# Optimization experiments

Hardware: AMD Instinct MI355X
Metric: run time of the kernel (lower is better)

## Reference

```python
import jax, jax.numpy as jnp
import numpy as np

NUM_HEADS = 8
NUM_LEVEL = 4
KERNEL = 2
NUM_POINT = KERNEL * KERNEL
D_MODEL = 256
HEAD_DIM = D_MODEL // NUM_HEADS
REF_SIZE = 4
EPS = 1e-6


def _kernel_indices():
    # even kernel: linspace(-k/2+0.5, k/2-0.5, k) -> [-0.5, 0.5] for k=2
    ind = np.linspace(-KERNEL // 2 + 0.5, KERNEL // 2 - 0.5, KERNEL)
    i, j = np.meshgrid(ind, ind, indexing='ij')
    ki = np.stack([j, i], axis=-1).reshape(-1, 2) / KERNEL  # (P, 2), (x, y)
    return jnp.asarray(ki, dtype=jnp.float32)


def _ref_windows(shapes):
    # mask is None -> centers on a regular grid, size = ref_size / (H, W)
    refs = []
    for (H, W) in shapes:
        y = (jnp.arange(1, H + 1, dtype=jnp.float32) - 0.5) / (H + EPS)
        x = (jnp.arange(1, W + 1, dtype=jnp.float32) - 0.5) / (W + EPS)
        yy, xx = jnp.meshgrid(y, x, indexing='ij')           # (H, W)
        center = jnp.stack([xx, yy], axis=-1).reshape(-1, 2)  # (HW, 2)
        size = jnp.broadcast_to(
            jnp.array([REF_SIZE / W, REF_SIZE / H], dtype=jnp.float32), center.shape)
        refs.append(jnp.concatenate([center, size], axis=-1))
    return jnp.concatenate(refs, axis=0)  # (L, 4)


def _bilinear_sample(vflat, grid, H, W):
    """vflat: (B, H*W, M, D) one level; grid: (B, Lq, M, P, 2) normalized [0,1].
    Returns (B, Lq, M, P, D). Zero padding outside, align_corners=False."""
    B, _, M, D = vflat.shape
    x = grid[..., 0] * W - 0.5
    y = grid[..., 1] * H - 0.5
    x0 = jnp.floor(x); y0 = jnp.floor(y)
    lx = x - x0; ly = y - y0
    x0i = x0.astype(jnp.int32); y0i = y0.astype(jnp.int32)
    bidx = jnp.arange(B)[:, None, None, None]
    midx = jnp.arange(M)[None, None, :, None]

    def corner(xi, yi, w):
        valid = (xi >= 0) & (xi < W) & (yi >= 0) & (yi < H)
        idx = jnp.clip(yi, 0, H - 1) * W + jnp.clip(xi, 0, W - 1)
        g = vflat[bidx, idx, midx]  # (B, Lq, M, P, D)
        return g * (w * valid.astype(w.dtype))[..., None]

    out = corner(x0i, y0i, (1 - lx) * (1 - ly))
    out = out + corner(x0i + 1, y0i, lx * (1 - ly))
    out = out + corner(x0i, y0i + 1, (1 - lx) * ly)
    out = out + corner(x0i + 1, y0i + 1, lx * ly)
    return out


def setup_inputs() -> dict:
    key = jax.random.key(0)
    ks = jax.random.split(key, 20)
    spatial = [(100, 100), (50, 50), (25, 25), (13, 13)]
    B = 4
    inp = {}
    for i, (H, W) in enumerate(spatial):
        inp[f'value{i}'] = jax.random.normal(ks[i], (B, D_MODEL, H, W), dtype=jnp.float32)
        inp[f'pos{i}'] = jax.random.normal(ks[4 + i], (B, D_MODEL, H, W), dtype=jnp.float32)
    s = 0.05
    inp['Wv'] = jax.random.normal(ks[8], (D_MODEL, D_MODEL), dtype=jnp.float32) * s
    inp['bv'] = jnp.zeros((D_MODEL,), dtype=jnp.float32)
    inp['Wo'] = jax.random.normal(ks[9], (D_MODEL, D_MODEL), dtype=jnp.float32) * s
    inp['bo'] = jnp.zeros((D_MODEL,), dtype=jnp.float32)
    nb = NUM_LEVEL * NUM_HEADS * 4
    inp['Wbox'] = jax.random.normal(ks[10], (nb, D_MODEL), dtype=jnp.float32) * s
    inp['bbox'] = jax.random.uniform(ks[11], (nb,), dtype=jnp.float32)
    na = NUM_HEADS * NUM_LEVEL * NUM_POINT
    inp['Wattn'] = jax.random.normal(ks[12], (na, D_MODEL), dtype=jnp.float32) * s
    inp['battn'] = jax.random.normal(ks[13], (na,), dtype=jnp.float32) * s
    return inp


def reference(value0, value1, value2, value3, pos0, pos1, pos2, pos3,
              Wv, bv, Wo, bo, Wbox, bbox, Wattn, battn):
    levels = [value0, value1, value2, value3]
    poss = [pos0, pos1, pos2, pos3]
    shapes = [(v.shape[2], v.shape[3]) for v in levels]
    B = levels[0].shape[0]

    # flatten pyramid: (B, C, H, W) -> (B, HW, C)
    value = jnp.concatenate(
        [v.reshape(B, D_MODEL, -1).transpose(0, 2, 1) for v in levels], axis=1)
    pos = jnp.concatenate(
        [p.reshape(B, D_MODEL, -1).transpose(0, 2, 1) for p in poss], axis=1)
    L = value.shape[1]

    query = value + pos
    vp = (value @ Wv.T + bv).reshape(B, L, NUM_HEADS, HEAD_DIM)

    attn = jax.nn.softmax(
        (query @ Wattn.T + battn).reshape(B, L, NUM_HEADS, NUM_LEVEL * NUM_POINT),
        axis=-1).reshape(B, L, NUM_HEADS, NUM_LEVEL, NUM_POINT)

    offset = (query @ Wbox.T + bbox).reshape(B, L, NUM_HEADS, NUM_LEVEL, 4)
    ref = _ref_windows(shapes)[None, :, None, None, :]          # (1, L, 1, 1, 4)
    boxes = ref + offset / 8.0 * ref[..., jnp.array([2, 3, 2, 3])]
    center = boxes[..., None, :2]                               # (B, L, M, NL, 1, 2)
    size = boxes[..., None, 2:]
    ki = _kernel_indices()[None, None, None, None, :, :]        # (1,1,1,1,P,2)
    grid = center + ki * jax.nn.relu(size)                      # (B, L, M, NL, P, 2)

    out = jnp.zeros((B, L, NUM_HEADS, HEAD_DIM), dtype=vp.dtype)
    start = 0
    for l, (H, W) in enumerate(shapes):
        end = start + H * W
        vf = vp[:, start:end]                                   # (B, HW, M, D)
        sampled = _bilinear_sample(vf, grid[:, :, :, l], H, W)  # (B, L, M, P, D)
        out = out + jnp.einsum('blmp,blmpd->blmd', attn[:, :, :, l], sampled)
        start = end

    return out.reshape(B, L, D_MODEL) @ Wo.T + bo
```

## Files before the change

### kernel.cpp

```cpp
#include <hip/hip_runtime.h>
#include <cstdint>
#include <cmath>

#define D_MODEL 256
#define NH 8
#define NLVL 4
#define LTOT 13294
#define BATCH 4
#define BTOT (BATCH * LTOT)
#define RPAD 53248

typedef __attribute__((ext_vector_type(8))) short bf8;
typedef __attribute__((ext_vector_type(4))) float f4;
typedef __attribute__((ext_vector_type(2))) float f2;

__device__ __forceinline__ unsigned short f2bf(float x) {
    unsigned u = __float_as_uint(x);
    u += 0x7fffu + ((u >> 16) & 1u);
    return (unsigned short)(u >> 16);
}
__device__ __forceinline__ float bf2f(unsigned short h) {
    return __uint_as_float(((unsigned)h) << 16);
}
__device__ __forceinline__ f2 up2(unsigned u) {
    return (f2){__uint_as_float(u << 16), __uint_as_float(u & 0xffff0000u)};
}
__device__ __forceinline__ int swzf(int i, int s) { return s ^ ((i >> 1) & 3); }

__device__ __forceinline__ void level_of(int l, int& lv, int& hw, int& Wl, int& HWl, int& loff) {
    if (l < 10000)      { lv = 0; loff = 0;     Wl = 100; HWl = 10000; }
    else if (l < 12500) { lv = 1; loff = 10000; Wl = 50;  HWl = 2500;  }
    else if (l < 13125) { lv = 2; loff = 12500; Wl = 25;  HWl = 625;   }
    else                { lv = 3; loff = 13125; Wl = 13;  HWl = 169;   }
    hw = l - loff;
}

__global__ __launch_bounds__(256) void pack_weights(
    const float* __restrict__ Wv, const float* __restrict__ Wattn,
    const float* __restrict__ Wbox, const float* __restrict__ Wo,
    unsigned short* __restrict__ W1hi, unsigned short* __restrict__ W1lo,
    unsigned short* __restrict__ Wohi, unsigned short* __restrict__ Wolo) {
    int tid = blockIdx.x * 256 + threadIdx.x;
    const float* src;
    unsigned short *dh, *dl;
    int nb, kb, j, s;
    if (tid < 16384) {
        nb = tid >> 12; kb = (tid >> 9) & 7; j = (tid >> 2) & 127; s = tid & 3;
        int f = nb * 128 + j, c0 = kb * 32 + s * 8;
        if (f < 256)      src = Wv + (size_t)f * 256 + c0;
        else if (f < 384) src = Wattn + (size_t)(f - 256) * 256 + c0;
        else              src = Wbox + (size_t)(f - 384) * 256 + c0;
        dh = W1hi; dl = W1lo;
    } else if (tid < 24576) {
        int t2 = tid - 16384;
        nb = t2 >> 12; kb = (t2 >> 9) & 7; j = (t2 >> 2) & 127; s = t2 & 3;
        int f = nb * 128 + j, c0 = kb * 32 + s * 8;
        src = Wo + (size_t)f * 256 + c0;
        dh = Wohi; dl = Wolo;
    } else return;
    int base = (((nb * 8 + kb) * 128 + j) * 4 + swzf(j, s)) * 8;
    #pragma unroll
    for (int e = 0; e < 8; ++e) {
        float x = src[e];
        unsigned short h = f2bf(x);
        dh[base + e] = h;
        dl[base + e] = f2bf(x - bf2f(h));
    }
}

__global__ __launch_bounds__(256) void convert_A(
    const float* __restrict__ v0, const float* __restrict__ v1,
    const float* __restrict__ v2, const float* __restrict__ v3,
    const float* __restrict__ p0, const float* __restrict__ p1,
    const float* __restrict__ p2, const float* __restrict__ p3,
    unsigned short* __restrict__ Gv, unsigned short* __restrict__ Gq) {
    __shared__ unsigned short HV[64][130];
    __shared__ unsigned short HQ[64][130];
    int t = threadIdx.x;
    int w = t >> 6, lane = t & 63;
    int r0 = blockIdx.x * 64;

    int r = r0 + lane; if (r >= BTOT) r = BTOT - 1;
    int b = r / LTOT, l = r % LTOT;
    int lv, hw, Wl, HWl, loff;
    level_of(l, lv, hw, Wl, HWl, loff);
    const float *vb, *pb;
    switch (lv) { case 0: vb = v0; pb = p0; break; case 1: vb = v1; pb = p1; break;
                  case 2: vb = v2; pb = p2; break; default: vb = v3; pb = p3; break; }
    size_t base = (size_t)b * D_MODEL * (size_t)HWl + (size_t)hw;
    vb += base; pb += base;

    int kb2 = (lane >> 2) & 3, slot = lane & 3;
    for (int h = 0; h < 2; ++h) {
        #pragma unroll 4
        for (int i = 0; i < 32; ++i) {
            int cl = i * 4 + w;
            int c = h * 128 + cl;
            float av = vb[(size_t)c * HWl];
            float aq = av + pb[(size_t)c * HWl];
            HV[lane][cl] = f2bf(av);
            HQ[lane][cl] = f2bf(aq);
        }
        __syncthreads();
        #pragma unroll
        for (int j = 0; j < 8; ++j) {
            int plane = j >> 2;
            int rl = (j & 3) * 16 + w * 4 + (lane >> 4);
            int oct = slot ^ ((rl >> 1) & 3);
            const unsigned* s32 = (const unsigned*)(plane ? &HQ[rl][kb2 * 32 + oct * 8]
                                                          : &HV[rl][kb2 * 32 + oct * 8]);
            uint4 vst = make_uint4(s32[0], s32[1], s32[2], s32[3]);
            unsigned short* dst = (plane ? Gq : Gv)
                + (size_t)(r0 + rl) * 256 + (h * 4 + kb2) * 32 + slot * 8;
            *(uint4*)dst = vst;
        }
        __syncthreads();
    }
}

__global__ __launch_bounds__(256) void gemm1_mfma(
    const unsigned short* __restrict__ Gv, const unsigned short* __restrict__ Gq,
    const unsigned short* __restrict__ W1hi, const unsigned short* __restrict__ W1lo,
    const float* __restrict__ bv, const float* __restrict__ battn, const float* __restrict__ bbox,
    unsigned short* __restrict__ VPb, float* __restrict__ LB) {
    __shared__ __align__(16) unsigned short Ah[2][4096], Bh[2][4096], Bl[2][4096];
    int t = threadIdx.x;
    int nb = blockIdx.x;
    int r0 = blockIdx.y * 128;
    const unsigned short* Asrc = (nb < 2) ? Gv : Gq;
    int w = t >> 6, lane = t & 63;
    int wr = w >> 1, wc = w & 1;
    int row_l = lane & 15, oct = lane >> 4;

    const unsigned short* Bbh = W1hi + (size_t)nb * 32768;
    const unsigned short* Bbl = W1lo + (size_t)nb * 32768;

    f4 acc[4][4];
    #pragma unroll
    for (int i = 0; i < 4; ++i)
        #pragma unroll
        for (int j = 0; j < 4; ++j) acc[i][j] = (f4){0.f, 0.f, 0.f, 0.f};

    int c0 = w * 64 + lane, c1 = c0 + 256;
    const unsigned short* a0b = Asrc + (size_t)(r0 + (c0 >> 2)) * 256 + (c0 & 3) * 8;
    const unsigned short* a1b = Asrc + (size_t)(r0 + (c1 >> 2)) * 256 + (c1 & 3) * 8;

#define G1_STAGE(bb, kb)                                                            \
    {                                                                               \
        __builtin_amdgcn_global_load_lds(a0b + (kb) * 32, &Ah[bb][w * 512], 16, 0, 0);        \
        __builtin_amdgcn_global_load_lds(a1b + (kb) * 32, &Ah[bb][2048 + w * 512], 16, 0, 0); \
        __builtin_amdgcn_global_load_lds(Bbh + (kb) * 4096 + c0 * 8, &Bh[bb][w * 512], 16, 0, 0);        \
        __builtin_amdgcn_global_load_lds(Bbh + (kb) * 4096 + c1 * 8, &Bh[bb][2048 + w * 512], 16, 0, 0); \
        __builtin_amdgcn_global_load_lds(Bbl + (kb) * 4096 + c0 * 8, &Bl[bb][w * 512], 16, 0, 0);        \
        __builtin_amdgcn_global_load_lds(Bbl + (kb) * 4096 + c1 * 8, &Bl[bb][2048 + w * 512], 16, 0, 0); \
    }

    G1_STAGE(0, 0);
    for (int kb = 0; kb < 8; ++kb) {
        __syncthreads();
        if (kb < 7) G1_STAGE((kb + 1) & 1, kb + 1);
        int bb = kb & 1;
        bf8 a[4], bh[4], bl[4];
        #pragma unroll
        for (int x = 0; x < 4; ++x) {
            int ri = wr * 64 + x * 16 + row_l;
            int ci = wc * 64 + x * 16 + row_l;
            a[x]  = *(const bf8*)(&Ah[bb][ri * 32 + swzf(ri, oct) * 8]);
            bh[x] = *(const bf8*)(&Bh[bb][ci * 32 + swzf(ci, oct) * 8]);
            bl[x] = *(const bf8*)(&Bl[bb][ci * 32 + swzf(ci, oct) * 8]);
        }
        #pragma unroll
        for (int mi = 0; mi < 4; ++mi)
            #pragma unroll
            for (int ni = 0; ni < 4; ++ni) {
                f4 c = acc[mi][ni];
                c = __builtin_amdgcn_mfma_f32_16x16x32_bf16(a[mi], bh[ni], c, 0, 0, 0);
                c = __builtin_amdgcn_mfma_f32_16x16x32_bf16(a[mi], bl[ni], c, 0, 0, 0);
                acc[mi][ni] = c;
            }
    }
    #pragma unroll
    for (int ni = 0; ni < 4; ++ni) {
        int col = wc * 64 + ni * 16 + row_l;
        float bias;
        if (nb == 0) bias = bv[col];
        else if (nb == 1) bias = bv[128 + col];
        else if (nb == 2) bias = battn[col];
        else bias = bbox[col];
        #pragma unroll
        for (int mi = 0; mi < 4; ++mi) {
            #pragma unroll
            for (int v = 0; v < 4; ++v) {
                int rr = r0 + wr * 64 + mi * 16 + oct * 4 + v;
                if (rr < BTOT) {
                    float val = acc[mi][ni][v] + bias;
                    if (nb < 2) VPb[(size_t)rr * 256 + nb * 128 + col] = f2bf(val);
                    else        LB[(size_t)rr * 256 + (nb - 2) * 128 + col] = val;
                }
            }
        }
    }
}

__global__ __launch_bounds__(256) void sampler_kernel(const unsigned short* __restrict__ VPb,
                                                      const float* __restrict__ LB,
                                                      unsigned short* __restrict__ att_hi,
                                                      unsigned short* __restrict__ att_lo) {
    __shared__ float sw[64][132];
    const int Ws2[4]   = {100, 50, 25, 13};
    const int offs2[4] = {0, 10000, 12500, 13125};
    int t = threadIdx.x;
    int blk = blockIdx.x;

    #pragma unroll
    for (int pass = 0; pass < 4; ++pass) {
        int g = (t >> 4) + pass * 16;
        int p = t & 15;
        int grp = blk * 64 + g;
        int m = grp & 7;
        int r = grp >> 3;
        int l = r % LTOT;
        int rb0 = r - l;

        int lv, hw, Wl, HWl, loff;
        level_of(l, lv, hw, Wl, HWl, loff);
        int x, y;
        switch (lv) {
            case 0:  y = hw / 100; x = hw - y * 100; break;
            case 1:  y = hw / 50;  x = hw - y * 50;  break;
            case 2:  y = hw / 25;  x = hw - y * 25;  break;
            default: y = hw / 13;  x = hw - y * 13;  break;
        }
        float denom = (float)((double)Wl + 1e-6);
        float cx = ((float)x + 0.5f) / denom;
        float cy = ((float)y + 0.5f) / denom;
        float rsw = 4.0f / (float)Wl;

        const float* Lrow = LB + (size_t)r * 256;
        float lg = Lrow[m * 16 + p];
        float mx = lg;
        #pragma unroll
        for (int off = 8; off >= 1; off >>= 1)
            mx = fmaxf(mx, __shfl_xor(mx, off, 16));
        float e = __expf(lg - mx);
        float ssum = e;
        #pragma unroll
        for (int off = 8; off >= 1; off >>= 1)
            ssum += __shfl_xor(ssum, off, 16);
        float aw = e / ssum;

        int lp = p >> 2, pp = p & 3;
        int W2 = Ws2[lp];
        float fW2 = (float)W2;
        float o0 = Lrow[128 + m * 16 + lp * 4 + 0];
        float o1 = Lrow[128 + m * 16 + lp * 4 + 1];
        float o2 = Lrow[128 + m * 16 + lp * 4 + 2];
        float o3 = Lrow[128 + m * 16 + lp * 4 + 3];
        float bcx = cx + o0 * 0.125f * rsw;
        float bcy = cy + o1 * 0.125f * rsw;
        float bsx = fmaxf(fmaf(o2 * 0.125f, rsw, rsw), 0.f);
        float bsy = fmaxf(fmaf(o3 * 0.125f, rsw, rsw), 0.f);
        float kx = (pp & 1)  ? 0.25f : -0.25f;
        float ky = (pp >> 1) ? 0.25f : -0.25f;
        float xs = fmaf(bcx + kx * bsx, fW2, -0.5f);
        float ys = fmaf(bcy + ky * bsy, fW2, -0.5f);
        float x0f = floorf(xs), y0f = floorf(ys);
        float lx = xs - x0f, ly = ys - y0f;
        int x0 = (int)x0f, y0 = (int)y0f;
        int x1 = x0 + 1, y1 = y0 + 1;
        bool vx0 = (x0 >= 0) & (x0 < W2), vx1 = (x1 >= 0) & (x1 < W2);
        bool vy0 = (y0 >= 0) & (y0 < W2), vy1 = (y1 >= 0) & (y1 < W2);
        int x0c = min(max(x0, 0), W2 - 1), x1c = min(max(x1, 0), W2 - 1);
        int y0c = min(max(y0, 0), W2 - 1), y1c = min(max(y1, 0), W2 - 1);
        float w00 = (vx0 & vy0) ? aw * (1.f - lx) * (1.f - ly) : 0.f;
        float w01 = (vx1 & vy0) ? aw * lx * (1.f - ly) : 0.f;
        float w10 = (vx0 & vy1) ? aw * (1.f - lx) * ly : 0.f;
        float w11 = (vx1 & vy1) ? aw * lx * ly : 0.f;
        int rowb = rb0 + offs2[lp];
        int col  = m * 32;
        int i00 = ((rowb + y0c * W2 + x0c) * 256 + col) * 2;
        int i01 = ((rowb + y0c * W2 + x1c) * 256 + col) * 2;
        int i10 = ((rowb + y1c * W2 + x0c) * 256 + col) * 2;
        int i11 = ((rowb + y1c * W2 + x1c) * 256 + col) * 2;
        float* dst = &sw[g][p * 8];
        *(float4*)dst       = (float4){w00, w01, w10, w11};
        *(float4*)(dst + 4) = (float4){__int_as_float(i00), __int_as_float(i01),
                                       __int_as_float(i10), __int_as_float(i11)};
    }
    __syncthreads();

    int g = t >> 2, lane4 = t & 3;
    unsigned dby = (unsigned)lane4 * 16u;
    const char* Vb = (const char*)VPb;
    f2 a01 = {0.f, 0.f}, a23 = {0.f, 0.f}, a45 = {0.f, 0.f}, a67 = {0.f, 0.f};
    #pragma unroll
    for (int p = 0; p < 16; ++p) {
        const float* sp = &sw[g][p * 8];
        float4 wv = *(const float4*)sp;
        float4 fi = *(const float4*)(sp + 4);
        uint4 u00 = *(const uint4*)(Vb + (size_t)(__float_as_uint(fi.x) + dby));
        uint4 u01 = *(const uint4*)(Vb + (size_t)(__float_as_uint(fi.y) + dby));
        uint4 u10 = *(const uint4*)(Vb + (size_t)(__float_as_uint(fi.z) + dby));
        uint4 u11 = *(const uint4*)(Vb + (size_t)(__float_as_uint(fi.w) + dby));
        f2 w0 = {wv.x, wv.x}, w1 = {wv.y, wv.y}, w2 = {wv.z, wv.z}, w3 = {wv.w, wv.w};
        a01 = __builtin_elementwise_fma(w0, up2(u00.x), a01);
        a23 = __builtin_elementwise_fma(w0, up2(u00.y), a23);
        a45 = __builtin_elementwise_fma(w0, up2(u00.z), a45);
        a67 = __builtin_elementwise_fma(w0, up2(u00.w), a67);
        a01 = __builtin_elementwise_fma(w1, up2(u01.x), a01);
        a23 = __builtin_elementwise_fma(w1, up2(u01.y), a23);
        a45 = __builtin_elementwise_fma(w1, up2(u01.z), a45);
        a67 = __builtin_elementwise_fma(w1, up2(u01.w), a67);
        a01 = __builtin_elementwise_fma(w2, up2(u10.x), a01);
        a23 = __builtin_elementwise_fma(w2, up2(u10.y), a23);
        a45 = __builtin_elementwise_fma(w2, up2(u10.z), a45);
        a67 = __builtin_elementwise_fma(w2, up2(u10.w), a67);
        a01 = __builtin_elementwise_fma(w3, up2(u11.x), a01);
        a23 = __builtin_elementwise_fma(w3, up2(u11.y), a23);
        a45 = __builtin_elementwise_fma(w3, up2(u11.z), a45);
        a67 = __builtin_elementwise_fma(w3, up2(u11.w), a67);
    }
    int grp = blk * 64 + g;
    int m2 = grp & 7, r2 = grp >> 3;
    int slot = lane4 ^ ((r2 >> 1) & 3);
    size_t base = (size_t)r2 * 256 + m2 * 32 + slot * 8;
    float av[8] = {a01.x, a01.y, a23.x, a23.y, a45.x, a45.y, a67.x, a67.y};
    unsigned hp[4], lp4[4];
    #pragma unroll
    for (int q = 0; q < 4; ++q) {
        unsigned short h0 = f2bf(av[q * 2]), h1 = f2bf(av[q * 2 + 1]);
        unsigned short l0 = f2bf(av[q * 2] - bf2f(h0)), l1 = f2bf(av[q * 2 + 1] - bf2f(h1));
        hp[q]  = ((unsigned)h1 << 16) | h0;
        lp4[q] = ((unsigned)l1 << 16) | l0;
    }
    *(uint4*)&att_hi[base] = make_uint4(hp[0], hp[1], hp[2], hp[3]);
    *(uint4*)&att_lo[base] = make_uint4(lp4[0], lp4[1], lp4[2], lp4[3]);
}

__global__ __launch_bounds__(256) void gemm2_mfma(
    const unsigned short* __restrict__ Ahi_g, const unsigned short* __restrict__ Alo_g,
    const unsigned short* __restrict__ Wohi, const unsigned short* __restrict__ Wolo,
    const float* __restrict__ bo, float* __restrict__ out) {
    __shared__ __align__(16) unsigned short Ah[2][4096], Al[2][4096], Bh[2][4096], Bl[2][4096];
    int t = threadIdx.x;
    int nb = blockIdx.x;
    int r0 = blockIdx.y * 128;
    int w = t >> 6, lane = t & 63;
    int wr = w >> 1, wc = w & 1;
    int row_l = lane & 15, oct = lane >> 4;

    const unsigned short* Bbh = Wohi + (size_t)nb * 32768;
    const unsigned short* Bbl = Wolo + (size_t)nb * 32768;

    f4 acc[4][4];
    #pragma unroll
    for (int i = 0; i < 4; ++i)
        #pragma unroll
        for (int j = 0; j < 4; ++j) acc[i][j] = (f4){0.f, 0.f, 0.f, 0.f};

    int c0 = w * 64 + lane, c1 = c0 + 256;
    int ra0 = r0 + (c0 >> 2); if (ra0 >= BTOT) ra0 = BTOT - 1;
    int ra1 = r0 + (c1 >> 2); if (ra1 >= BTOT) ra1 = BTOT - 1;
    const unsigned short* ah0 = Ahi_g + (size_t)ra0 * 256 + (c0 & 3) * 8;
    const unsigned short* ah1 = Ahi_g + (size_t)ra1 * 256 + (c1 & 3) * 8;
    const unsigned short* al0 = Alo_g + (size_t)ra0 * 256 + (c0 & 3) * 8;
    const unsigned short* al1 = Alo_g + (size_t)ra1 * 256 + (c1 & 3) * 8;

#define G2_STAGE(bb, kb)                                                            \
    {                                                                               \
        __builtin_amdgcn_global_load_lds(ah0 + (kb) * 32, &Ah[bb][w * 512], 16, 0, 0);        \
        __builtin_amdgcn_global_load_lds(ah1 + (kb) * 32, &Ah[bb][2048 + w * 512], 16, 0, 0); \
        __builtin_amdgcn_global_load_lds(al0 + (kb) * 32, &Al[bb][w * 512], 16, 0, 0);        \
        __builtin_amdgcn_global_load_lds(al1 + (kb) * 32, &Al[bb][2048 + w * 512], 16, 0, 0); \
        __builtin_amdgcn_global_load_lds(Bbh + (kb) * 4096 + c0 * 8, &Bh[bb][w * 512], 16, 0, 0);        \
        __builtin_amdgcn_global_load_lds(Bbh + (kb) * 4096 + c1 * 8, &Bh[bb][2048 + w * 512], 16, 0, 0); \
        __builtin_amdgcn_global_load_lds(Bbl + (kb) * 4096 + c0 * 8, &Bl[bb][w * 512], 16, 0, 0);        \
        __builtin_amdgcn_global_load_lds(Bbl + (kb) * 4096 + c1 * 8, &Bl[bb][2048 + w * 512], 16, 0, 0); \
    }

    G2_STAGE(0, 0);
    for (int kb = 0; kb < 8; ++kb) {
        __syncthreads();
        if (kb < 7) G2_STAGE((kb + 1) & 1, kb + 1);
        int bb = kb & 1;
        bf8 ah[4], al[4], bh[4], bl[4];
        #pragma unroll
        for (int x = 0; x < 4; ++x) {
            int ri = wr * 64 + x * 16 + row_l;
            int ci = wc * 64 + x * 16 + row_l;
            ah[x] = *(const bf8*)(&Ah[bb][ri * 32 + swzf(ri, oct) * 8]);
            al[x] = *(const bf8*)(&Al[bb][ri * 32 + swzf(ri, oct) * 8]);
            bh[x] = *(const bf8*)(&Bh[bb][ci * 32 + swzf(ci, oct) * 8]);
            bl[x] = *(const bf8*)(&Bl[bb][ci * 32 + swzf(ci, oct) * 8]);
        }
        #pragma unroll
        for (int mi = 0; mi < 4; ++mi)
            #pragma unroll
            for (int ni = 0; ni < 4; ++ni) {
                f4 c = acc[mi][ni];
                c = __builtin_amdgcn_mfma_f32_16x16x32_bf16(ah[mi], bh[ni], c, 0, 0, 0);
                c = __builtin_amdgcn_mfma_f32_16x16x32_bf16(ah[mi], bl[ni], c, 0, 0, 0);
                c = __builtin_amdgcn_mfma_f32_16x16x32_bf16(al[mi], bh[ni], c, 0, 0, 0);
                acc[mi][ni] = c;
            }
    }
    #pragma unroll
    for (int ni = 0; ni < 4; ++ni) {
        int col = wc * 64 + ni * 16 + row_l;
        float bias = bo[nb * 128 + col];
        #pragma unroll
        for (int mi = 0; mi < 4; ++mi) {
            #pragma unroll
            for (int v = 0; v < 4; ++v) {
                int rr = r0 + wr * 64 + mi * 16 + oct * 4 + v;
                if (rr < BTOT)
                    out[(size_t)rr * 256 + nb * 128 + col] = acc[mi][ni][v] + bias;
            }
        }
    }
}

extern "C" void kernel_launch(void* const* d_in, const int* in_sizes, int n_in,
                              void* d_out, int out_size, void* d_ws, size_t ws_size,
                              hipStream_t stream) {
    const float* v0 = (const float*)d_in[0];
    const float* p0 = (const float*)d_in[1];
    const float* v1 = (const float*)d_in[2];
    const float* p1 = (const float*)d_in[3];
    const float* v2 = (const float*)d_in[4];
    const float* p2 = (const float*)d_in[5];
    const float* v3 = (const float*)d_in[6];
    const float* p3 = (const float*)d_in[7];
    const float* Wv    = (const float*)d_in[8];
    const float* bv    = (const float*)d_in[9];
    const float* Wo    = (const float*)d_in[10];
    const float* bo    = (const float*)d_in[11];
    const float* Wbox  = (const float*)d_in[12];
    const float* bbox  = (const float*)d_in[13];
    const float* Wattn = (const float*)d_in[14];
    const float* battn = (const float*)d_in[15];
    float* out = (float*)d_out;

    char* ws = (char*)d_ws;
    unsigned short* W1hi = (unsigned short*)(ws);
    unsigned short* W1lo = (unsigned short*)(ws + 262144);
    unsigned short* Wohi = (unsigned short*)(ws + 524288);
    unsigned short* Wolo = (unsigned short*)(ws + 655360);
    unsigned short* Gv   = (unsigned short*)(ws + 1048576);
    unsigned short* Gq   = (unsigned short*)(ws + 1048576 + 27262976);
    unsigned short* atth = Gv;
    unsigned short* attl = Gq;
    unsigned short* VPb  = (unsigned short*)(ws + 1048576 + 2 * 27262976);
    float*          LB   = (float*)(ws + 1048576 + 2 * 27262976 + 27226112);

    convert_A<<<dim3(RPAD / 64), dim3(256), 0, stream>>>(v0, v1, v2, v3,
                                                         p0, p1, p2, p3, Gv, Gq);
    pack_weights<<<dim3(96), dim3(256), 0, stream>>>(Wv, Wattn, Wbox, Wo,
                                                     W1hi, W1lo, Wohi, Wolo);

    gemm1_mfma<<<dim3(4, RPAD / 128), dim3(256), 0, stream>>>(
        Gv, Gq, W1hi, W1lo, bv, battn, bbox, VPb, LB);

    sampler_kernel<<<dim3((BTOT * NH) / 64), dim3(256), 0, stream>>>(VPb, LB, atth, attl);

    gemm2_mfma<<<dim3(2, (BTOT + 127) / 128), dim3(256), 0, stream>>>(
        atth, attl, Wohi, Wolo, bo, out);
}
```

Baseline: 237.4 us.

## Add XCD-aware block swizzle to GEMMs and sampler; widen sampler to 512 threads

Flattens the GEMM grids to 1D and remaps block IDs so consecutive logical tiles land on the same XCD, improving L2 locality for shared A rows and weight tiles. The sampler gets the same remap so neighbouring query groups, which gather overlapping value rows, share an XCD L2. The sampler also moves to 512 threads per block: each thread now gathers 8 bytes per corner instead of 16, with 8 lanes per head group, which raises memory-level parallelism at the cost of narrower loads. Launch bounds request 8 blocks per CU, which may cap registers.

New measurement: 253.7 us. 1.07x slower.

```diff
diff --git a/kernel.cpp b/kernel.cpp
--- a/kernel.cpp
+++ b/kernel.cpp
@@ -26,6 +26,11 @@
     return (f2){__uint_as_float(u << 16), __uint_as_float(u & 0xffff0000u)};
 }
 __device__ __forceinline__ int swzf(int i, int s) { return s ^ ((i >> 1) & 3); }
+__device__ __forceinline__ int xcd_swz(int hw, int nwg) {
+    int xcd = hw & 7, k = hw >> 3;
+    int q = nwg >> 3, r = nwg & 7;
+    return (xcd < r ? xcd * (q + 1) : r * (q + 1) + (xcd - r) * q) + k;
+}
 
 __device__ __forceinline__ void level_of(int l, int& lv, int& hw, int& Wl, int& HWl, int& loff) {
     if (l < 10000)      { lv = 0; loff = 0;     Wl = 100; HWl = 10000; }
@@ -125,8 +130,9 @@
     unsigned short* __restrict__ VPb, float* __restrict__ LB) {
     __shared__ __align__(16) unsigned short Ah[2][4096], Bh[2][4096], Bl[2][4096];
     int t = threadIdx.x;
-    int nb = blockIdx.x;
-    int r0 = blockIdx.y * 128;
+    int lid = xcd_swz(blockIdx.x, 4 * (RPAD / 128));
+    int nb = lid & 3;
+    int r0 = (lid >> 2) * 128;
     const unsigned short* Asrc = (nb < 2) ? Gv : Gq;
     int w = t >> 6, lane = t & 63;
     int wr = w >> 1, wc = w & 1;
@@ -202,19 +208,19 @@
     }
 }
 
-__global__ __launch_bounds__(256) void sampler_kernel(const unsigned short* __restrict__ VPb,
-                                                      const float* __restrict__ LB,
-                                                      unsigned short* __restrict__ att_hi,
-                                                      unsigned short* __restrict__ att_lo) {
+__global__ __launch_bounds__(512, 8) void sampler_kernel(const unsigned short* __restrict__ VPb,
+                                                         const float* __restrict__ LB,
+                                                         unsigned short* __restrict__ att_hi,
+                                                         unsigned short* __restrict__ att_lo) {
     __shared__ float sw[64][132];
     const int Ws2[4]   = {100, 50, 25, 13};
     const int offs2[4] = {0, 10000, 12500, 13125};
     int t = threadIdx.x;
-    int blk = blockIdx.x;
-
-    #pragma unroll
-    for (int pass = 0; pass < 4; ++pass) {
-        int g = (t >> 4) + pass * 16;
+    int blk = xcd_swz(blockIdx.x, (BTOT * NH) / 64);
+
+    #pragma unroll
+    for (int pass = 0; pass < 2; ++pass) {
+        int g = (t >> 4) + pass * 32;
         int p = t & 15;
         int grp = blk * 64 + g;
         int m = grp & 7;
@@ -289,52 +295,45 @@
     }
     __syncthreads();
 
-    int g = t >> 2, lane4 = t & 3;
-    unsigned dby = (unsigned)lane4 * 16u;
+    int g = t >> 3, lane8 = t & 7;
+    unsigned dby = (unsigned)lane8 * 8u;
     const char* Vb = (const char*)VPb;
-    f2 a01 = {0.f, 0.f}, a23 = {0.f, 0.f}, a45 = {0.f, 0.f}, a67 = {0.f, 0.f};
+    f2 a01 = {0.f, 0.f}, a23 = {0.f, 0.f};
     #pragma unroll
     for (int p = 0; p < 16; ++p) {
         const float* sp = &sw[g][p * 8];
         float4 wv = *(const float4*)sp;
         float4 fi = *(const float4*)(sp + 4);
-        uint4 u00 = *(const uint4*)(Vb + (size_t)(__float_as_uint(fi.x) + dby));
-        uint4 u01 = *(const uint4*)(Vb + (size_t)(__float_as_uint(fi.y) + dby));
-        uint4 u10 = *(const uint4*)(Vb + (size_t)(__float_as_uint(fi.z) + dby));
-        uint4 u11 = *(const uint4*)(Vb + (size_t)(__float_as_uint(fi.w) + dby));
+        uint2 u00 = *(const uint2*)(Vb + (size_t)(__float_as_uint(fi.x) + dby));
+        uint2 u01 = *(const uint2*)(Vb + (size_t)(__float_as_uint(fi.y) + dby));
+        uint2 u10 = *(const uint2*)(Vb + (size_t)(__float_as_uint(fi.z) + dby));
+        uint2 u11 = *(const uint2*)(Vb + (size_t)(__float_as_uint(fi.w) + dby));
         f2 w0 = {wv.x, wv.x}, w1 = {wv.y, wv.y}, w2 = {wv.z, wv.z}, w3 = {wv.w, wv.w};
         a01 = __builtin_elementwise_fma(w0, up2(u00.x), a01);
         a23 = __builtin_elementwise_fma(w0, up2(u00.y), a23);
-        a45 = __builtin_elementwise_fma(w0, up2(u00.z), a45);
-        a67 = __builtin_elementwise_fma(w0, up2(u00.w), a67);
         a01 = __builtin_elementwise_fma(w1, up2(u01.x), a01);
         a23 = __builtin_elementwise_fma(w1, up2(u01.y), a23);
-        a45 = __builtin_elementwise_fma(w1, up2(u01.z), a45);
-        a67 = __builtin_elementwise_fma(w1, up2(u01.w), a67);
         a01 = __builtin_elementwise_fma(w2, up2(u10.x), a01);
         a23 = __builtin_elementwise_fma(w2, up2(u10.y), a23);
-        a45 = __builtin_elementwise_fma(w2, up2(u10.z), a45);
-        a67 = __builtin_elementwise_fma(w2, up2(u10.w), a67);
         a01 = __builtin_elementwise_fma(w3, up2(u11.x), a01);
         a23 = __builtin_elementwise_fma(w3, up2(u11.y), a23);
-        a45 = __builtin_elementwise_fma(w3, up2(u11.z), a45);
-        a67 = __builtin_elementwise_fma(w3, up2(u11.w), a67);
     }
     int grp = blk * 64 + g;
     int m2 = grp & 7, r2 = grp >> 3;
-    int slot = lane4 ^ ((r2 >> 1) & 3);
-    size_t base = (size_t)r2 * 256 + m2 * 32 + slot * 8;
-    float av[8] = {a01.x, a01.y, a23.x, a23.y, a45.x, a45.y, a67.x, a67.y};
-    unsigned hp[4], lp4[4];
-    #pragma unroll
-    for (int q = 0; q < 4; ++q) {
+    int d0 = lane8 * 4;
+    int slot = (d0 >> 3) ^ ((r2 >> 1) & 3);
+    size_t base = (size_t)r2 * 256 + m2 * 32 + slot * 8 + (d0 & 7);
+    float av[4] = {a01.x, a01.y, a23.x, a23.y};
+    unsigned hp[2], lp2[2];
+    #pragma unroll
+    for (int q = 0; q < 2; ++q) {
         unsigned short h0 = f2bf(av[q * 2]), h1 = f2bf(av[q * 2 + 1]);
         unsigned short l0 = f2bf(av[q * 2] - bf2f(h0)), l1 = f2bf(av[q * 2 + 1] - bf2f(h1));
         hp[q]  = ((unsigned)h1 << 16) | h0;
-        lp4[q] = ((unsigned)l1 << 16) | l0;
-    }
-    *(uint4*)&att_hi[base] = make_uint4(hp[0], hp[1], hp[2], hp[3]);
-    *(uint4*)&att_lo[base] = make_uint4(lp4[0], lp4[1], lp4[2], lp4[3]);
+        lp2[q] = ((unsigned)l1 << 16) | l0;
+    }
+    *(uint2*)&att_hi[base] = make_uint2(hp[0], hp[1]);
+    *(uint2*)&att_lo[base] = make_uint2(lp2[0], lp2[1]);
 }
 
 __global__ __launch_bounds__(256) void gemm2_mfma(
@@ -343,8 +342,9 @@
     const float* __restrict__ bo, float* __restrict__ out) {
     __shared__ __align__(16) unsigned short Ah[2][4096], Al[2][4096], Bh[2][4096], Bl[2][4096];
     int t = threadIdx.x;
-    int nb = blockIdx.x;
-    int r0 = blockIdx.y * 128;
+    int lid = xcd_swz(blockIdx.x, 2 * ((BTOT + 127) / 128));
+    int nb = lid & 1;
+    int r0 = (lid >> 1) * 128;
     int w = t >> 6, lane = t & 63;
     int wr = w >> 1, wc = w & 1;
     int row_l = lane & 15, oct = lane >> 4;
@@ -458,11 +458,11 @@
     pack_weights<<<dim3(96), dim3(256), 0, stream>>>(Wv, Wattn, Wbox, Wo,
                                                      W1hi, W1lo, Wohi, Wolo);
 
-    gemm1_mfma<<<dim3(4, RPAD / 128), dim3(256), 0, stream>>>(
+    gemm1_mfma<<<dim3(4 * (RPAD / 128)), dim3(256), 0, stream>>>(
         Gv, Gq, W1hi, W1lo, bv, battn, bbox, VPb, LB);
 
-    sampler_kernel<<<dim3((BTOT * NH) / 64), dim3(256), 0, stream>>>(VPb, LB, atth, attl);
-
-    gemm2_mfma<<<dim3(2, (BTOT + 127) / 128), dim3(256), 0, stream>>>(
+    sampler_kernel<<<dim3((BTOT * NH) / 64), dim3(512), 0, stream>>>(VPb, LB, atth, attl);
+
+    gemm2_mfma<<<dim3(2 * ((BTOT + 127) / 128)), dim3(256), 0, stream>>>(
         atth, attl, Wohi, Wolo, bo, out);
 }
```
